# Optimization experiments

Measured on AMD Instinct MI355X. Metric: run time of the kernel, lower is better.

The kernel has to match this reference:

```python
import jax, jax.numpy as jnp
import numpy as np
import math

D_MODEL = 1024
N_HEADS = 16
C = 1
B, L = 8, 2048


def _glorot(key, fan):
    lim = np.sqrt(6.0 / (fan + fan)).astype(np.float32)
    return jax.random.uniform(key, (fan, fan), jnp.float32, -lim, lim)


def setup_inputs() -> dict:
    key = jax.random.key(0)
    ks = jax.random.split(key, 7)
    queries = jax.random.normal(ks[0], (B, L, D_MODEL), jnp.float32)
    keys = jax.random.normal(ks[1], (B, L, D_MODEL), jnp.float32)
    values = jax.random.normal(ks[2], (B, L, D_MODEL), jnp.float32)
    wq = _glorot(ks[3], D_MODEL)
    wk = _glorot(ks[4], D_MODEL)
    wv = _glorot(ks[5], D_MODEL)
    wo = _glorot(ks[6], D_MODEL)
    return {"queries": queries, "keys": keys, "values": values,
            "wq": wq, "wk": wk, "wv": wv, "wo": wo}


def reference(queries, keys, values, wq, wk, wv, wo):
    Bv, Lv, _ = queries.shape
    H = N_HEADS
    Dh = D_MODEL // N_HEADS
    # Projections, then (B, L, H, Dh) -> (B, H, Dh, L)  (time axis last)
    Q = (queries @ wq).reshape(Bv, Lv, H, Dh).transpose(0, 2, 3, 1)
    K = (keys @ wk).reshape(Bv, Lv, H, Dh).transpose(0, 2, 3, 1)
    V = (values @ wv).reshape(Bv, Lv, H, Dh).transpose(0, 2, 3, 1)
    # FFT-based autocorrelation over the time axis, per (B,H,Dh) lane
    corr = jnp.fft.irfft(jnp.fft.rfft(Q, axis=-1) * jnp.conj(jnp.fft.rfft(K, axis=-1)), n=Lv, axis=-1)  # (B,H,Dh,L)
    k_top = int(math.floor(C * math.log(Lv)))
    top_vals, top_idx = jax.lax.top_k(corr, k_top)          # (B,H,Dh,k)
    w = jax.nn.softmax(top_vals, axis=-1)                    # (B,H,Dh,k)
    # Faithful to original roll_function: it rolls along the Dh axis
    # (which the source mislabels as seq_len), shifts taken mod Dh.
    # out[b,h,t,:] = V[b,h,(t - tau[b,h,t]) % Dh, :]
    t = jnp.arange(Dh)
    out = jnp.zeros_like(V)
    for i in range(k_top):  # small static loop (k_top = 7)
        gather_idx = (t[None, None, :] - top_idx[..., i]) % Dh   # (B,H,Dh)
        rolled = jnp.take_along_axis(V, gather_idx[..., None], axis=2)  # (B,H,Dh,L)
        out = out + w[..., i, None] * rolled
    # Faithful layout-scrambling reshape: (B,H,Dh,L)->(B,Dh,H,L)->(B,L,d_model)
    out = out.transpose(0, 2, 1, 3).reshape(Bv, Lv, D_MODEL)
    return out @ wo
```

## Files before the change

### kernel.cpp

```cpp
#include <hip/hip_runtime.h>
#include <math.h>

#define NB 8
#define NL 2048
#define ND 1024
#define NH 16
#define KTOP 7

typedef __attribute__((ext_vector_type(4))) float f32x4;
typedef __attribute__((ext_vector_type(8))) short s16x8;
typedef __attribute__((ext_vector_type(8))) _Float16 f16x8;
typedef __attribute__((ext_vector_type(4))) _Float16 f16x4;

__device__ __forceinline__ unsigned short f2bf(float x) {
  unsigned u = __float_as_uint(x);
  u = (u + 0x7FFFu + ((u >> 16) & 1u)) >> 16;
  return (unsigned short)u;
}
__device__ __forceinline__ float bf2f(unsigned short h) {
  return __uint_as_float(((unsigned)h) << 16);
}
__device__ __forceinline__ void gll16(const void* g, void* l) {
  __builtin_amdgcn_global_load_lds(
      (const __attribute__((address_space(1))) void*)g,
      (__attribute__((address_space(3))) void*)l, 16, 0, 0);
}

__global__ __launch_bounds__(256) void wprep_kernel(
    const float* __restrict__ w0, const float* __restrict__ w1,
    const float* __restrict__ w2, const float* __restrict__ w3,
    short* __restrict__ wsplit,
    _Float16* __restrict__ wf16)
{
  __shared__ float tile[32][33];
  int y = blockIdx.y;
  const float* in = (y == 0) ? w0 : (y == 1) ? w1 : (y == 2) ? w2 : w3;
  int bx = blockIdx.x & 31, by = blockIdx.x >> 5;
  int tx = threadIdx.x & 31, ty = threadIdx.x >> 5;
#pragma unroll
  for (int i = 0; i < 4; ++i)
    tile[ty + i * 8][tx] = in[(size_t)(by * 32 + ty + i * 8) * ND + bx * 32 + tx];
  __syncthreads();
#pragma unroll
  for (int i = 0; i < 4; ++i) {
    float x = tile[tx][ty + i * 8];
    int n = bx * 32 + ty + i * 8;
    int k = by * 32 + tx;
    if (y < 2) {
      short* oh = wsplit + (size_t)(2 * y) * ND * ND;
      short* ol = wsplit + (size_t)(2 * y + 1) * ND * ND;
      unsigned short h = f2bf(x);
      unsigned short l = f2bf(x - bf2f(h));
      size_t o = (size_t)n * ND + (k ^ ((n & 3) << 3));
      oh[o] = (short)h;
      ol[o] = (short)l;
    } else {
      _Float16* of = wf16 + (size_t)(y - 2) * ND * ND;
      of[(size_t)n * ND + (k ^ ((n & 7) << 3))] = (_Float16)x;
    }
  }
}

__global__ __launch_bounds__(256) void gemm_split(
    const float* __restrict__ A, const short* __restrict__ BhT,
    const short* __restrict__ BlT, float* __restrict__ Ct) {
  constexpr int K = 1024;
  __shared__ short ah[4096], al[4096], bh[4096], bl[4096];
  int t = threadIdx.x;
  int wg = (blockIdx.x & 7) * 128 + (blockIdx.x >> 3);
  int m0 = (wg >> 3) << 7, n0 = (wg & 7) << 7;
  int lane = t & 63;
  int wm = (t >> 7) & 1, wn = (t >> 6) & 1;
  int lrow = lane & 15, lk8 = (lane >> 4) << 3;

  f32x4 acc[4][4] = {};

  for (int k0 = 0; k0 < K; k0 += 32) {
#pragma unroll
    for (int it = 0; it < 2; ++it) {
      int cb = it * 256 + t;
      int r = cb >> 2, c8 = (cb & 3) << 3;
      int lo = it * 2048 + (t & 192) * 8;
      gll16(BhT + (size_t)(n0 + r) * K + k0 + c8, bh + lo);
      gll16(BlT + (size_t)(n0 + r) * K + k0 + c8, bl + lo);
    }
#pragma unroll
    for (int it = 0; it < 2; ++it) {
      int ca = it * 256 + t;
      int r = ca >> 2, c8 = (ca & 3) << 3;
      const float* pa = A + (size_t)(m0 + r) * K + k0 + c8;
      float4 x = *(const float4*)pa;
      float4 y = *(const float4*)(pa + 4);
      float v[8] = {x.x, x.y, x.z, x.w, y.x, y.y, y.z, y.w};
      s16x8 hv, lv;
#pragma unroll
      for (int j = 0; j < 8; ++j) {
        unsigned short h = f2bf(v[j]);
        hv[j] = (short)h;
        lv[j] = (short)(unsigned short)(__float_as_uint(v[j] - bf2f(h)) >> 16);
      }
      int wi = r * 32 + (c8 ^ ((r & 3) << 3));
      *(s16x8*)(ah + wi) = hv;
      *(s16x8*)(al + wi) = lv;
    }
    __syncthreads();

    s16x8 afh[4], afl[4];
#pragma unroll
    for (int mf = 0; mf < 4; ++mf) {
      int row = wm * 64 + mf * 16 + lrow;
      int idx = row * 32 + (lk8 ^ ((row & 3) << 3));
      afh[mf] = *(const s16x8*)(ah + idx);
      afl[mf] = *(const s16x8*)(al + idx);
    }
#pragma unroll
    for (int nf = 0; nf < 4; ++nf) {
      int row = wn * 64 + nf * 16 + lrow;
      int idx = row * 32 + (lk8 ^ ((row & 3) << 3));
      s16x8 bfh = *(const s16x8*)(bh + idx);
      s16x8 bfl = *(const s16x8*)(bl + idx);
#pragma unroll
      for (int mf = 0; mf < 4; ++mf) {
        acc[mf][nf] = __builtin_amdgcn_mfma_f32_16x16x32_bf16(afh[mf], bfh, acc[mf][nf], 0, 0, 0);
        acc[mf][nf] = __builtin_amdgcn_mfma_f32_16x16x32_bf16(afh[mf], bfl, acc[mf][nf], 0, 0, 0);
        acc[mf][nf] = __builtin_amdgcn_mfma_f32_16x16x32_bf16(afl[mf], bfh, acc[mf][nf], 0, 0, 0);
      }
    }
    __syncthreads();
  }

  int b = m0 >> 11;
  int mlbase = (m0 & 2047) + wm * 64 + (lane >> 4) * 4;
#pragma unroll
  for (int nf = 0; nf < 4; ++nf) {
    int n = n0 + wn * 64 + nf * 16 + lrow;
    float* rowp = Ct + ((size_t)(b * ND + n)) * NL + mlbase;
#pragma unroll
    for (int mf = 0; mf < 4; ++mf)
      *(float4*)(rowp + mf * 16) = *(float4*)&acc[mf][nf];
  }
}

template <int OUTMODE, bool AF32>
__global__ __launch_bounds__(256) void gemm_f16(
    const void* __restrict__ Av, const _Float16* __restrict__ BT,
    void* __restrict__ Cv) {
  constexpr int K = 1024;
  __shared__ _Float16 sA[8192];
  __shared__ _Float16 sB[8192];
  int t = threadIdx.x;
  int wg = (blockIdx.x & 7) * 128 + (blockIdx.x >> 3);
  int m0 = (wg >> 3) << 7, n0 = (wg & 7) << 7;
  int lane = t & 63;
  int wm = (t >> 7) & 1, wn = (t >> 6) & 1;
  int lrow = lane & 15, lk = (lane >> 4) << 3;

  f32x4 acc[4][4] = {};

  for (int k0 = 0; k0 < K; k0 += 64) {
#pragma unroll
    for (int it = 0; it < 4; ++it) {
      int e = it * 256 + t;
      int r = e >> 3, c8 = (e & 7) << 3;
      int lo = it * 2048 + (t & 192) * 8;
      gll16(BT + (size_t)(n0 + r) * K + k0 + c8, sB + lo);
      if (!AF32) {
        const _Float16* Af = (const _Float16*)Av;
        gll16(Af + (size_t)(m0 + r) * K + k0 + c8, sA + lo);
      }
    }
    if (AF32) {
      const float* Af = (const float*)Av;
#pragma unroll
      for (int it = 0; it < 4; ++it) {
        int ca = it * 256 + t;
        int r = ca >> 3, c8 = (ca & 7) << 3;
        const float* pa = Af + (size_t)(m0 + r) * K + k0 + c8;
        float4 x = *(const float4*)pa;
        float4 y = *(const float4*)(pa + 4);
        f16x8 o;
        o[0] = (_Float16)x.x; o[1] = (_Float16)x.y; o[2] = (_Float16)x.z; o[3] = (_Float16)x.w;
        o[4] = (_Float16)y.x; o[5] = (_Float16)y.y; o[6] = (_Float16)y.z; o[7] = (_Float16)y.w;
        *(f16x8*)(sA + r * 64 + (c8 ^ ((r & 7) << 3))) = o;
      }
    }
    __syncthreads();
#pragma unroll
    for (int kk = 0; kk < 64; kk += 32) {
      f16x8 af[4];
#pragma unroll
      for (int mf = 0; mf < 4; ++mf) {
        int row = wm * 64 + mf * 16 + lrow;
        af[mf] = *(const f16x8*)(sA + row * 64 + ((kk + lk) ^ ((row & 7) << 3)));
      }
#pragma unroll
      for (int nf = 0; nf < 4; ++nf) {
        int row = wn * 64 + nf * 16 + lrow;
        f16x8 bf = *(const f16x8*)(sB + row * 64 + ((kk + lk) ^ ((row & 7) << 3)));
#pragma unroll
        for (int mf = 0; mf < 4; ++mf)
          acc[mf][nf] = __builtin_amdgcn_mfma_f32_16x16x32_f16(af[mf], bf, acc[mf][nf], 0, 0, 0);
      }
    }
    __syncthreads();
  }

  if (OUTMODE == 0) {
    _Float16* C = (_Float16*)Cv;
    int b = m0 >> 11;
    int ml = (m0 & 2047) + wm * 64 + (lane >> 4) * 4;
#pragma unroll
    for (int nf = 0; nf < 4; ++nf) {
      int n = n0 + wn * 64 + nf * 16 + lrow;
      _Float16* row = C + ((size_t)(b * ND + n)) * NL + ml;
#pragma unroll
      for (int mf = 0; mf < 4; ++mf) {
        f16x4 v;
        v[0] = (_Float16)acc[mf][nf][0];
        v[1] = (_Float16)acc[mf][nf][1];
        v[2] = (_Float16)acc[mf][nf][2];
        v[3] = (_Float16)acc[mf][nf][3];
        *(f16x4*)(row + mf * 16) = v;
      }
    }
  } else {
    float* C = (float*)Cv;
#pragma unroll
    for (int mf = 0; mf < 4; ++mf)
#pragma unroll
      for (int nf = 0; nf < 4; ++nf) {
        int row = m0 + wm * 64 + mf * 16 + (lane >> 4) * 4;
        int col = n0 + wn * 64 + nf * 16 + lrow;
#pragma unroll
        for (int r = 0; r < 4; ++r)
          C[(size_t)(row + r) * ND + col] = acc[mf][nf][r];
      }
  }
}

__device__ __forceinline__ int SW(int i) { return i ^ ((i >> 4) & 7); }

__device__ __forceinline__ float2 cadd2(float2 a, float2 b) { return make_float2(a.x + b.x, a.y + b.y); }
__device__ __forceinline__ float2 csub2(float2 a, float2 b) { return make_float2(a.x - b.x, a.y - b.y); }
__device__ __forceinline__ float2 cmul2(float2 a, float2 b) {
  return make_float2(a.x * b.x - a.y * b.y, a.x * b.y + a.y * b.x);
}
__device__ __forceinline__ float2 cjs2(float2 a, float s) { return make_float2(-s * a.y, s * a.x); }

__device__ __forceinline__ void dft4(float2& b0, float2& b1, float2& b2, float2& b3, float s) {
  float2 t0 = cadd2(b0, b2), t1 = csub2(b0, b2);
  float2 t2 = cadd2(b1, b3), t3 = cjs2(csub2(b1, b3), s);
  b0 = cadd2(t0, t2);
  b1 = cadd2(t1, t3);
  b2 = csub2(t0, t2);
  b3 = csub2(t1, t3);
}

__device__ __forceinline__ void dft8(float2 a[8], float s) {
  float2 e0 = a[0], e1 = a[2], e2 = a[4], e3 = a[6];
  float2 o0 = a[1], o1 = a[3], o2 = a[5], o3 = a[7];
  dft4(e0, e1, e2, e3, s);
  dft4(o0, o1, o2, o3, s);
  const float c = 0.70710678118654752f;
  float2 w1 = make_float2(c, s * c);
  float2 w3 = make_float2(-c, s * c);
  o1 = cmul2(o1, w1);
  o2 = cjs2(o2, s);
  o3 = cmul2(o3, w3);
  a[0] = cadd2(e0, o0);
  a[4] = csub2(e0, o0);
  a[1] = cadd2(e1, o1);
  a[5] = csub2(e1, o1);
  a[2] = cadd2(e2, o2);
  a[6] = csub2(e2, o2);
  a[3] = cadd2(e3, o3);
  a[7] = csub2(e3, o3);
}

template <int LS>
__device__ __forceinline__ void pass8(const float2* __restrict__ in, float2* __restrict__ out,
                                      float s, int t) {
  int k = t & (LS - 1);
  int blk = t / LS;
  float2 a[8];
#pragma unroll
  for (int r = 0; r < 8; ++r) a[r] = in[SW(t + 256 * r)];
  if (LS > 1) {
    float ang = s * (6.283185307179586f / (float)(LS * 8)) * (float)k;
    float2 w;
    sincosf(ang, &w.y, &w.x);
    float2 wr = w;
    a[1] = cmul2(a[1], wr);
#pragma unroll
    for (int r = 2; r < 8; ++r) {
      wr = cmul2(wr, w);
      a[r] = cmul2(a[r], wr);
    }
  }
  dft8(a, s);
  int ob = blk * (LS * 8) + k;
#pragma unroll
  for (int r = 0; r < 8; ++r) out[SW(ob + LS * r)] = a[r];
}

__global__ __launch_bounds__(256) void fft_topk_kernel(
    const float* __restrict__ Qt, const float* __restrict__ Kt,
    float* __restrict__ topw, int* __restrict__ topi) {
  __shared__ float2 X[2048];
  __shared__ float2 Y[2048];
  __shared__ float cv[4];
  __shared__ int ct[4];

  int t = threadIdx.x;
  size_t rix = blockIdx.x;
  const float* q = Qt + rix * NL;
  const float* k = Kt + rix * NL;

#pragma unroll
  for (int it = 0; it < 2; ++it) {
    int i0 = 4 * t + 1024 * it;
    float4 vq = *(const float4*)(q + i0);
    float4 vk = *(const float4*)(k + i0);
    X[SW(i0 + 0)] = make_float2(vq.x, vk.x);
    X[SW(i0 + 1)] = make_float2(vq.y, vk.y);
    X[SW(i0 + 2)] = make_float2(vq.z, vk.z);
    X[SW(i0 + 3)] = make_float2(vq.w, vk.w);
  }
  __syncthreads();

  pass8<1>(X, Y, -1.0f, t);
  __syncthreads();
  pass8<8>(Y, X, -1.0f, t);
  __syncthreads();
  pass8<64>(X, Y, -1.0f, t);
  __syncthreads();
#pragma unroll
  for (int h = 0; h < 2; ++h) {
    int b = t + 256 * h;
    float2 a[4];
#pragma unroll
    for (int r = 0; r < 4; ++r) a[r] = Y[SW(b + 512 * r)];
    float ang = -(6.283185307179586f / 2048.0f) * (float)b;
    float2 w;
    sincosf(ang, &w.y, &w.x);
    a[1] = cmul2(a[1], w);
    float2 w2 = cmul2(w, w);
    a[2] = cmul2(a[2], w2);
    a[3] = cmul2(a[3], cmul2(w2, w));
    dft4(a[0], a[1], a[2], a[3], -1.0f);
#pragma unroll
    for (int r = 0; r < 4; ++r) X[SW(b + 512 * r)] = a[r];
  }
  __syncthreads();

#pragma unroll
  for (int it = 0; it < 8; ++it) {
    int f = t + 256 * it;
    int nf = (2048 - f) & 2047;
    float2 zf = X[SW(f)];
    float2 zn = X[SW(nf)];
    float a = zf.x, b2 = zf.y, c = zn.x, d = zn.y;
    float p = 0.5f * (a + c), qq = 0.5f * (b2 - d);
    float r2 = 0.5f * (b2 + d), s2 = -0.5f * (a - c);
    Y[SW(f)] = make_float2((p * r2 + qq * s2) * (1.0f / 2048.0f),
                           (qq * r2 - p * s2) * (1.0f / 2048.0f));
  }
  __syncthreads();

  pass8<1>(Y, X, 1.0f, t);
  __syncthreads();
  pass8<8>(X, Y, 1.0f, t);
  __syncthreads();
  pass8<64>(Y, X, 1.0f, t);
  __syncthreads();

  float lv[8];
  int lt[8];
#pragma unroll
  for (int h = 0; h < 2; ++h) {
    int b = t + 256 * h;
    float2 a[4];
#pragma unroll
    for (int r = 0; r < 4; ++r) a[r] = X[SW(b + 512 * r)];
    float ang = (6.283185307179586f / 2048.0f) * (float)b;
    float2 w;
    sincosf(ang, &w.y, &w.x);
    a[1] = cmul2(a[1], w);
    float2 w2 = cmul2(w, w);
    a[2] = cmul2(a[2], w2);
    a[3] = cmul2(a[3], cmul2(w2, w));
    dft4(a[0], a[1], a[2], a[3], 1.0f);
#pragma unroll
    for (int r = 0; r < 4; ++r) {
      lv[h * 4 + r] = a[r].x;
      lt[h * 4 + r] = b + 512 * r;
    }
  }

  int lane = t & 63, wave = t >> 6;
  float sel_v[KTOP];
  int sel_t[KTOP];
#pragma unroll
  for (int pass = 0; pass < KTOP; ++pass) {
    float bv = -3.0e38f;
    int bt = 0x7FFFFFFF;
#pragma unroll
    for (int j = 0; j < 8; ++j)
      if (lv[j] > bv || (lv[j] == bv && lt[j] < bt)) { bv = lv[j]; bt = lt[j]; }
#pragma unroll
    for (int m = 1; m < 64; m <<= 1) {
      float ov = __shfl_xor(bv, m, 64);
      int ot = __shfl_xor(bt, m, 64);
      if (ov > bv || (ov == bv && ot < bt)) { bv = ov; bt = ot; }
    }
    if (lane == 0) { cv[wave] = bv; ct[wave] = bt; }
    __syncthreads();
    float fv = cv[0];
    int ft = ct[0];
#pragma unroll
    for (int w = 1; w < 4; ++w) {
      float ov = cv[w];
      int ot = ct[w];
      if (ov > fv || (ov == fv && ot < ft)) { fv = ov; ft = ot; }
    }
    sel_v[pass] = fv;
    sel_t[pass] = ft;
#pragma unroll
    for (int j = 0; j < 8; ++j)
      if (lt[j] == ft) lv[j] = -3.0e38f;
    __syncthreads();
  }

  if (t == 0) {
    float m = sel_v[0], ssum = 0.f, w[KTOP];
#pragma unroll
    for (int i = 0; i < KTOP; ++i) { w[i] = expf(sel_v[i] - m); ssum += w[i]; }
#pragma unroll
    for (int i = 0; i < KTOP; ++i) {
      topw[rix * KTOP + i] = w[i] / ssum;
      topi[rix * KTOP + i] = sel_t[i];
    }
  }
}

__global__ __launch_bounds__(256) void roll_kernel(
    const _Float16* __restrict__ V, const float* __restrict__ topw,
    const int* __restrict__ topi, _Float16* __restrict__ out) {
  __shared__ float vt[64][68];
  __shared__ float ws[64][8];
  __shared__ int ts[64][8];
  int blk = blockIdx.x;
  int b = blk >> 9;
  int h = (blk >> 5) & 15;
  int lc = blk & 31;
  int t = threadIdx.x;

#pragma unroll
  for (int it = 0; it < 2; ++it) {
    int e = it * 256 + t;
    int d = e >> 3, c8 = (e & 7) << 3;
    f16x8 v = *(const f16x8*)(V + ((size_t)(b * ND + h * 64 + d)) * NL + lc * 64 + c8);
#pragma unroll
    for (int j = 0; j < 8; ++j) vt[d][c8 + j] = (float)v[j];
  }
  for (int e = t; e < 64 * KTOP; e += 256) {
    int d = e / KTOP, i = e % KTOP;
    size_t rix = ((size_t)(b * 16 + h)) * 64 + d;
    ws[d][i] = topw[rix * KTOP + i];
    ts[d][i] = topi[rix * KTOP + i] & 63;
  }
  __syncthreads();

  int hi = lc >> 4;
  int c0 = (lc & 15) * 64;
#pragma unroll
  for (int it = 0; it < 16; ++it) {
    int e = it * 256 + t;
    int d = e >> 6, r = e & 63;
    float s = 0.f;
#pragma unroll
    for (int i = 0; i < KTOP; ++i) s += ws[d][i] * vt[(d - ts[d][i]) & 63][r];
    int rowp = d * 32 + h * 2 + hi;
    int col = c0 + r;
    out[((size_t)(b * NL + rowp)) * ND + (col ^ ((rowp & 7) << 3))] = (_Float16)s;
  }
}

extern "C" void kernel_launch(void* const* d_in, const int* in_sizes, int n_in,
                              void* d_out, int out_size, void* d_ws, size_t ws_size,
                              hipStream_t stream) {
  (void)in_sizes; (void)n_in; (void)out_size; (void)ws_size;
  const float* queries = (const float*)d_in[0];
  const float* keys    = (const float*)d_in[1];
  const float* values  = (const float*)d_in[2];
  const float* wq = (const float*)d_in[3];
  const float* wk = (const float*)d_in[4];
  const float* wv = (const float*)d_in[5];
  const float* wo = (const float*)d_in[6];
  float* outp = (float*)d_out;

  const size_t MB = 1024 * 1024;
  char* ws = (char*)d_ws;
  short*    wsplit = (short*)ws;
  _Float16* wf16   = (_Float16*)(ws + 8 * MB);
  float*    Qt     = (float*)(ws + 12 * MB);
  float*    Kt     = (float*)(ws + 76 * MB);
  float*    topw   = (float*)(ws + 140 * MB);
  int*      topi   = (int*)(ws + 140 * MB + (size_t)8192 * KTOP * 4);

  short* wqh = wsplit + (size_t)0 * ND * ND;
  short* wql = wsplit + (size_t)1 * ND * ND;
  short* wkh = wsplit + (size_t)2 * ND * ND;
  short* wkl = wsplit + (size_t)3 * ND * ND;
  _Float16* wv16 = wf16 + (size_t)0 * ND * ND;
  _Float16* wo16 = wf16 + (size_t)1 * ND * ND;

  _Float16* Vp = (_Float16*)Qt;
  _Float16* Xs = (_Float16*)Kt;

  wprep_kernel<<<dim3(1024, 4), 256, 0, stream>>>(wq, wk, wv, wo, wsplit, wf16);

  gemm_split<<<1024, 256, 0, stream>>>(queries, wqh, wql, Qt);
  gemm_split<<<1024, 256, 0, stream>>>(keys, wkh, wkl, Kt);

  fft_topk_kernel<<<8192, 256, 0, stream>>>(Qt, Kt, topw, topi);

  gemm_f16<0, true><<<1024, 256, 0, stream>>>(values, wv16, Vp);

  roll_kernel<<<NB * NH * 32, 256, 0, stream>>>(Vp, topw, topi, Xs);

  gemm_f16<2, false><<<1024, 256, 0, stream>>>(Xs, wo16, outp);
}
```

Before: 545.0 us.

## Use packed bf16 converts, hardware sin/cos twiddles, and lighter top-k reduction

The GEMM A-split conversion now uses v_cvt_pk_bf16_f32 packed converts instead of manual rounding, and the MFMA calls are reordered into three independent loops. The FFT twiddles use the hardware sin/cos builtins instead of sincosf, with w4 computed directly to shorten the multiply chain. LDS swizzle indexing is simplified, and top-k drops the tie-break compares, double-buffers the per-wave scratch to remove one barrier per pass, and recomputes the local max only when the winner came from this thread. The hardware sin/cos and the dropped tie-break may change numerics or tie order slightly.

```diff
diff --git a/kernel.cpp b/kernel.cpp
--- a/kernel.cpp
+++ b/kernel.cpp
@@ -20,6 +20,14 @@
 __device__ __forceinline__ float bf2f(unsigned short h) {
   return __uint_as_float(((unsigned)h) << 16);
 }
+__device__ __forceinline__ unsigned cvtpk_bf16(float a, float b) {
+  unsigned d;
+  asm("v_cvt_pk_bf16_f32 %0, %1, %2" : "=v"(d) : "v"(a), "v"(b));
+  return d;
+}
+__device__ __forceinline__ float lo16(unsigned h) { return __uint_as_float(h << 16); }
+__device__ __forceinline__ float hi16(unsigned h) { return __uint_as_float(h & 0xffff0000u); }
+
 __device__ __forceinline__ void gll16(const void* g, void* l) {
   __builtin_amdgcn_global_load_lds(
       (const __attribute__((address_space(1))) void*)g,
@@ -29,9 +37,7 @@
 __global__ __launch_bounds__(256) void wprep_kernel(
     const float* __restrict__ w0, const float* __restrict__ w1,
     const float* __restrict__ w2, const float* __restrict__ w3,
-    short* __restrict__ wsplit,
-    _Float16* __restrict__ wf16)
-{
+    short* __restrict__ wsplit, _Float16* __restrict__ wf16) {
   __shared__ float tile[32][33];
   int y = blockIdx.y;
   const float* in = (y == 0) ? w0 : (y == 1) ? w1 : (y == 2) ? w2 : w3;
@@ -91,17 +97,21 @@
       const float* pa = A + (size_t)(m0 + r) * K + k0 + c8;
       float4 x = *(const float4*)pa;
       float4 y = *(const float4*)(pa + 4);
-      float v[8] = {x.x, x.y, x.z, x.w, y.x, y.y, y.z, y.w};
-      s16x8 hv, lv;
-#pragma unroll
-      for (int j = 0; j < 8; ++j) {
-        unsigned short h = f2bf(v[j]);
-        hv[j] = (short)h;
-        lv[j] = (short)(unsigned short)(__float_as_uint(v[j] - bf2f(h)) >> 16);
-      }
+      unsigned h0 = cvtpk_bf16(x.x, x.y);
+      unsigned h1 = cvtpk_bf16(x.z, x.w);
+      unsigned h2 = cvtpk_bf16(y.x, y.y);
+      unsigned h3 = cvtpk_bf16(y.z, y.w);
+      float r0 = x.x - lo16(h0), r1 = x.y - hi16(h0);
+      float r2 = x.z - lo16(h1), r3 = x.w - hi16(h1);
+      float r4 = y.x - lo16(h2), r5 = y.y - hi16(h2);
+      float r6 = y.z - lo16(h3), r7 = y.w - hi16(h3);
+      unsigned l0 = cvtpk_bf16(r0, r1);
+      unsigned l1 = cvtpk_bf16(r2, r3);
+      unsigned l2 = cvtpk_bf16(r4, r5);
+      unsigned l3 = cvtpk_bf16(r6, r7);
       int wi = r * 32 + (c8 ^ ((r & 3) << 3));
-      *(s16x8*)(ah + wi) = hv;
-      *(s16x8*)(al + wi) = lv;
+      *(uint4*)(ah + wi) = make_uint4(h0, h1, h2, h3);
+      *(uint4*)(al + wi) = make_uint4(l0, l1, l2, l3);
     }
     __syncthreads();
 
@@ -120,11 +130,14 @@
       s16x8 bfh = *(const s16x8*)(bh + idx);
       s16x8 bfl = *(const s16x8*)(bl + idx);
 #pragma unroll
-      for (int mf = 0; mf < 4; ++mf) {
+      for (int mf = 0; mf < 4; ++mf)
         acc[mf][nf] = __builtin_amdgcn_mfma_f32_16x16x32_bf16(afh[mf], bfh, acc[mf][nf], 0, 0, 0);
+#pragma unroll
+      for (int mf = 0; mf < 4; ++mf)
         acc[mf][nf] = __builtin_amdgcn_mfma_f32_16x16x32_bf16(afh[mf], bfl, acc[mf][nf], 0, 0, 0);
+#pragma unroll
+      for (int mf = 0; mf < 4; ++mf)
         acc[mf][nf] = __builtin_amdgcn_mfma_f32_16x16x32_bf16(afl[mf], bfh, acc[mf][nf], 0, 0, 0);
-      }
     }
     __syncthreads();
   }
@@ -246,6 +259,9 @@
   return make_float2(a.x * b.x - a.y * b.y, a.x * b.y + a.y * b.x);
 }
 __device__ __forceinline__ float2 cjs2(float2 a, float s) { return make_float2(-s * a.y, s * a.x); }
+__device__ __forceinline__ float2 wtw(float rev) {
+  return make_float2(__builtin_amdgcn_cosf(rev), __builtin_amdgcn_sinf(rev));
+}
 
 __device__ __forceinline__ void dft4(float2& b0, float2& b1, float2& b2, float2& b3, float s) {
   float2 t0 = cadd2(b0, b2), t1 = csub2(b0, b2);
@@ -280,25 +296,30 @@
 template <int LS>
 __device__ __forceinline__ void pass8(const float2* __restrict__ in, float2* __restrict__ out,
                                       float s, int t) {
+  float2 a[8];
+  const float2* ip = in + (t ^ ((t >> 4) & 7));
+#pragma unroll
+  for (int r = 0; r < 8; ++r) a[r] = ip[256 * r];
   int k = t & (LS - 1);
-  int blk = t / LS;
-  float2 a[8];
-#pragma unroll
-  for (int r = 0; r < 8; ++r) a[r] = in[SW(t + 256 * r)];
   if (LS > 1) {
-    float ang = s * (6.283185307179586f / (float)(LS * 8)) * (float)k;
-    float2 w;
-    sincosf(ang, &w.y, &w.x);
-    float2 wr = w;
-    a[1] = cmul2(a[1], wr);
-#pragma unroll
-    for (int r = 2; r < 8; ++r) {
-      wr = cmul2(wr, w);
-      a[r] = cmul2(a[r], wr);
-    }
+    float kf = s * (1.0f / (LS * 8)) * (float)k;
+    float2 w1 = wtw(kf);
+    float2 w4 = wtw(4.0f * kf);
+    float2 w2 = cmul2(w1, w1);
+    float2 w3 = cmul2(w2, w1);
+    float2 w5 = cmul2(w4, w1);
+    float2 w6 = cmul2(w4, w2);
+    float2 w7 = cmul2(w4, w3);
+    a[1] = cmul2(a[1], w1);
+    a[2] = cmul2(a[2], w2);
+    a[3] = cmul2(a[3], w3);
+    a[4] = cmul2(a[4], w4);
+    a[5] = cmul2(a[5], w5);
+    a[6] = cmul2(a[6], w6);
+    a[7] = cmul2(a[7], w7);
   }
   dft8(a, s);
-  int ob = blk * (LS * 8) + k;
+  int ob = (t / LS) * (LS * 8) + k;
 #pragma unroll
   for (int r = 0; r < 8; ++r) out[SW(ob + LS * r)] = a[r];
 }
@@ -308,8 +329,8 @@
     float* __restrict__ topw, int* __restrict__ topi) {
   __shared__ float2 X[2048];
   __shared__ float2 Y[2048];
-  __shared__ float cv[4];
-  __shared__ int ct[4];
+  __shared__ float cv[2][4];
+  __shared__ int ct[2][4];
 
   int t = threadIdx.x;
   size_t rix = blockIdx.x;
@@ -321,10 +342,11 @@
     int i0 = 4 * t + 1024 * it;
     float4 vq = *(const float4*)(q + i0);
     float4 vk = *(const float4*)(k + i0);
-    X[SW(i0 + 0)] = make_float2(vq.x, vk.x);
-    X[SW(i0 + 1)] = make_float2(vq.y, vk.y);
-    X[SW(i0 + 2)] = make_float2(vq.z, vk.z);
-    X[SW(i0 + 3)] = make_float2(vq.w, vk.w);
+    int swb = SW(i0);
+    X[swb ^ 0] = make_float2(vq.x, vk.x);
+    X[swb ^ 1] = make_float2(vq.y, vk.y);
+    X[swb ^ 2] = make_float2(vq.z, vk.z);
+    X[swb ^ 3] = make_float2(vq.w, vk.w);
   }
   __syncthreads();
 
@@ -338,18 +360,18 @@
   for (int h = 0; h < 2; ++h) {
     int b = t + 256 * h;
     float2 a[4];
-#pragma unroll
-    for (int r = 0; r < 4; ++r) a[r] = Y[SW(b + 512 * r)];
-    float ang = -(6.283185307179586f / 2048.0f) * (float)b;
-    float2 w;
-    sincosf(ang, &w.y, &w.x);
+    const float2* yp = Y + SW(b);
+#pragma unroll
+    for (int r = 0; r < 4; ++r) a[r] = yp[512 * r];
+    float2 w = wtw(-(1.0f / 2048.0f) * (float)b);
+    float2 w2 = cmul2(w, w);
     a[1] = cmul2(a[1], w);
-    float2 w2 = cmul2(w, w);
     a[2] = cmul2(a[2], w2);
     a[3] = cmul2(a[3], cmul2(w2, w));
     dft4(a[0], a[1], a[2], a[3], -1.0f);
-#pragma unroll
-    for (int r = 0; r < 4; ++r) X[SW(b + 512 * r)] = a[r];
+    float2* xp = X + SW(b);
+#pragma unroll
+    for (int r = 0; r < 4; ++r) xp[512 * r] = a[r];
   }
   __syncthreads();
 
@@ -357,13 +379,13 @@
   for (int it = 0; it < 8; ++it) {
     int f = t + 256 * it;
     int nf = (2048 - f) & 2047;
-    float2 zf = X[SW(f)];
+    float2 zf = X[SW(t) + 256 * it];
     float2 zn = X[SW(nf)];
     float a = zf.x, b2 = zf.y, c = zn.x, d = zn.y;
     float p = 0.5f * (a + c), qq = 0.5f * (b2 - d);
     float r2 = 0.5f * (b2 + d), s2 = -0.5f * (a - c);
-    Y[SW(f)] = make_float2((p * r2 + qq * s2) * (1.0f / 2048.0f),
-                           (qq * r2 - p * s2) * (1.0f / 2048.0f));
+    Y[SW(t) + 256 * it] = make_float2((p * r2 + qq * s2) * (1.0f / 2048.0f),
+                                      (qq * r2 - p * s2) * (1.0f / 2048.0f));
   }
   __syncthreads();
 
@@ -380,13 +402,12 @@
   for (int h = 0; h < 2; ++h) {
     int b = t + 256 * h;
     float2 a[4];
-#pragma unroll
-    for (int r = 0; r < 4; ++r) a[r] = X[SW(b + 512 * r)];
-    float ang = (6.283185307179586f / 2048.0f) * (float)b;
-    float2 w;
-    sincosf(ang, &w.y, &w.x);
+    const float2* xp = X + SW(b);
+#pragma unroll
+    for (int r = 0; r < 4; ++r) a[r] = xp[512 * r];
+    float2 w = wtw((1.0f / 2048.0f) * (float)b);
+    float2 w2 = cmul2(w, w);
     a[1] = cmul2(a[1], w);
-    float2 w2 = cmul2(w, w);
     a[2] = cmul2(a[2], w2);
     a[3] = cmul2(a[3], cmul2(w2, w));
     dft4(a[0], a[1], a[2], a[3], 1.0f);
@@ -398,37 +419,45 @@
   }
 
   int lane = t & 63, wave = t >> 6;
+  float bv = lv[0];
+  int bt = lt[0];
+#pragma unroll
+  for (int j = 1; j < 8; ++j)
+    if (lv[j] > bv) { bv = lv[j]; bt = lt[j]; }
+
   float sel_v[KTOP];
   int sel_t[KTOP];
 #pragma unroll
   for (int pass = 0; pass < KTOP; ++pass) {
-    float bv = -3.0e38f;
-    int bt = 0x7FFFFFFF;
-#pragma unroll
-    for (int j = 0; j < 8; ++j)
-      if (lv[j] > bv || (lv[j] == bv && lt[j] < bt)) { bv = lv[j]; bt = lt[j]; }
+    float rv = bv;
+    int rt = bt;
 #pragma unroll
     for (int m = 1; m < 64; m <<= 1) {
-      float ov = __shfl_xor(bv, m, 64);
-      int ot = __shfl_xor(bt, m, 64);
-      if (ov > bv || (ov == bv && ot < bt)) { bv = ov; bt = ot; }
-    }
-    if (lane == 0) { cv[wave] = bv; ct[wave] = bt; }
+      float ov = __shfl_xor(rv, m, 64);
+      int ot = __shfl_xor(rt, m, 64);
+      if (ov > rv) { rv = ov; rt = ot; }
+    }
+    if (lane == 0) { cv[pass & 1][wave] = rv; ct[pass & 1][wave] = rt; }
     __syncthreads();
-    float fv = cv[0];
-    int ft = ct[0];
+    float fv = cv[pass & 1][0];
+    int ft = ct[pass & 1][0];
 #pragma unroll
     for (int w = 1; w < 4; ++w) {
-      float ov = cv[w];
-      int ot = ct[w];
-      if (ov > fv || (ov == fv && ot < ft)) { fv = ov; ft = ot; }
+      float ov = cv[pass & 1][w];
+      if (ov > fv) { fv = ov; ft = ct[pass & 1][w]; }
     }
     sel_v[pass] = fv;
     sel_t[pass] = ft;
-#pragma unroll
-    for (int j = 0; j < 8; ++j)
-      if (lt[j] == ft) lv[j] = -3.0e38f;
-    __syncthreads();
+    if (bt == ft) {
+#pragma unroll
+      for (int j = 0; j < 8; ++j)
+        if (lt[j] == ft) lv[j] = -3.0e38f;
+      bv = lv[0];
+      bt = lt[0];
+#pragma unroll
+      for (int j = 1; j < 8; ++j)
+        if (lv[j] > bv) { bv = lv[j]; bt = lt[j]; }
+    }
   }
 
   if (t == 0) {
```

After: 493.6 us. 9.4% less time.
